# Performance work log

Hardware: AMD Instinct MI355X
Metric: run time of the kernel (lower is better)

## Reference

```python
import jax, jax.numpy as jnp
import numpy as np

D_MODEL = 2048
NUM_HEADS = 16
HEAD_DIM = D_MODEL // NUM_HEADS
B, S = 2, 2048


def rotate_half(x):
    x1, x2 = jnp.split(x, 2, axis=-1)
    return jnp.concatenate((-x2, x1), axis=-1)


def setup_inputs() -> dict:
    key = jax.random.key(0)
    ks = jax.random.split(key, 7)
    x = jax.random.normal(ks[0], (B, S, D_MODEL), dtype=jnp.float32)
    cos = jax.random.normal(ks[1], (1, 1, S, HEAD_DIM), dtype=jnp.float32)
    sin = jax.random.normal(ks[2], (1, 1, S, HEAD_DIM), dtype=jnp.float32)
    scale = 1.0 / np.sqrt(D_MODEL)
    Wq = jax.random.normal(ks[3], (D_MODEL, D_MODEL), dtype=jnp.float32) * scale
    Wk = jax.random.normal(ks[4], (D_MODEL, D_MODEL), dtype=jnp.float32) * scale
    Wv = jax.random.normal(ks[5], (D_MODEL, D_MODEL), dtype=jnp.float32) * scale
    Wo = jax.random.normal(ks[6], (D_MODEL, D_MODEL), dtype=jnp.float32) * scale
    return {"x": x, "cos": cos, "sin": sin, "Wq": Wq, "Wk": Wk, "Wv": Wv, "Wo": Wo}


def reference(x, cos, sin, Wq, Wk, Wv, Wo):
    Bb, Ss, Dd = x.shape
    H, hd = NUM_HEADS, HEAD_DIM
    # nn.Linear: y = x @ W.T ; here W stored as [out, in]
    q = (x @ Wq.T).reshape(Bb, Ss, H, hd).transpose(0, 2, 1, 3)  # [B,H,S,hd]
    k = (x @ Wk.T).reshape(Bb, Ss, H, hd).transpose(0, 2, 1, 3)
    v = (x @ Wv.T).reshape(Bb, Ss, H, hd).transpose(0, 2, 1, 3)
    q = q * cos + rotate_half(q) * sin
    k = k * cos + rotate_half(k) * sin
    scale = 1.0 / jnp.sqrt(jnp.asarray(hd, dtype=x.dtype))
    scores = jnp.einsum('bhqd,bhkd->bhqk', q, k) * scale  # [B,H,S,S]
    causal = jnp.tril(jnp.ones((Ss, Ss), dtype=bool))
    scores = jnp.where(causal[None, None], scores, jnp.finfo(x.dtype).min)
    attn = jax.nn.softmax(scores, axis=-1)
    out = jnp.einsum('bhqk,bhkd->bhqd', attn, v)  # [B,H,S,hd]
    out = out.transpose(0, 2, 1, 3).reshape(Bb, Ss, Dd)
    return out @ Wo.T
```

## Files before the change

### kernel.cpp

```cpp
#include <hip/hip_runtime.h>

typedef unsigned short u16;
typedef __attribute__((ext_vector_type(8))) short bf8v;
typedef __attribute__((ext_vector_type(4))) float f4v;

#define DEV static __device__ __forceinline__

DEV float bf2f(u16 u){ unsigned x = ((unsigned)u) << 16; float f; __builtin_memcpy(&f, &x, 4); return f; }
DEV u16 f2bf(float f){ unsigned x; __builtin_memcpy(&x, &f, 4); x += 0x7fff + ((x >> 16) & 1); return (u16)(x >> 16); }

DEV void async16(const void* g, void* l){
  __builtin_amdgcn_global_load_lds((const __attribute__((address_space(1))) unsigned*)g,
                                   (__attribute__((address_space(3))) unsigned*)l, 16, 0, 0);
}

DEV void vwait6(){ asm volatile("s_waitcnt vmcnt(6)" ::: "memory"); }
DEV void vwait0(){ asm volatile("s_waitcnt vmcnt(0)" ::: "memory"); }
DEV void bar(){ asm volatile("s_barrier" ::: "memory"); }

__global__ __launch_bounds__(256) void f2b_k(const float* __restrict__ src,
                                             u16* __restrict__ dst)
{
  const long i = ((long)blockIdx.x * 256 + threadIdx.x) * 4;
  const float4 v = *(const float4*)(src + i);
  ushort4 o;
  o.x = f2bf(v.x); o.y = f2bf(v.y); o.z = f2bf(v.z); o.w = f2bf(v.w);
  *(ushort4*)(dst + i) = o;
}

__global__ __launch_bounds__(256) void f2b3_k(const float* __restrict__ a,
                                              const float* __restrict__ b,
                                              const float* __restrict__ c,
                                              u16* __restrict__ dst)
{
  const int bx = blockIdx.x;
  const float* s = bx < 4096 ? a : (bx < 8192 ? b : c);
  const long soff = ((long)(bx & 4095) * 256 + threadIdx.x) * 4;
  const long doff = ((long)bx * 256 + threadIdx.x) * 4;
  const float4 v = *(const float4*)(s + soff);
  ushort4 o;
  o.x = f2bf(v.x); o.y = f2bf(v.y); o.z = f2bf(v.z); o.w = f2bf(v.w);
  *(ushort4*)(dst + doff) = o;
}

constexpr int KDIM = 2048;

__global__ __launch_bounds__(512, 2) void gemm256(const u16* __restrict__ A,
                                                  const u16* __restrict__ B,
                                                  u16* __restrict__ C0,
                                                  u16* __restrict__ C1,
                                                  u16* __restrict__ C2,
                                                  float* __restrict__ Cf, int mode)
{
  __shared__ __align__(16) u16 Asm[3][8192];
  __shared__ __align__(16) u16 Bsm[3][16384];

  const int tid = threadIdx.x;
  const int w = tid >> 6, lane = tid & 63;
  const int ln = lane & 15, quad = lane >> 4;
  const int wr = w >> 2, wc = w & 3;

  const int gx = gridDim.x;
  const int nwg = gx * gridDim.y;
  const int wg = blockIdx.y * gx + blockIdx.x;
  const int swz = (wg & 7) * (nwg >> 3) + (wg >> 3);
  const int bx = swz % gx, by = swz / gx;
  const long m0 = (long)by << 7, n0 = (long)bx << 8;

  f4v acc[4][4] = {};

  const u16* pA  = A + (m0 + w * 16 + ln) * (long)KDIM + quad * 8;
  const u16* pB0 = B + (n0 + w * 16 + ln) * (long)KDIM + quad * 8;
  const u16* pB1 = B + (n0 + (8 + w) * 16 + ln) * (long)KDIM + quad * 8;
  char* ldsA = (char*)Asm + (long)tid * 16;
  char* ldsB = (char*)Bsm + (long)tid * 16;

#define STG(sl, ks, kt) do{                                                     \
    async16(pA  + (kt) + (ks) * 32, ldsA + (sl) * 16384 + (ks) * 8192);         \
    async16(pB0 + (kt) + (ks) * 32, ldsB + (sl) * 32768 + (ks) * 16384);        \
    async16(pB1 + (kt) + (ks) * 32, ldsB + (sl) * 32768 + (ks) * 16384 + 8192); \
  }while(0)

  STG(0, 0, 0);  STG(0, 1, 0);
  STG(1, 0, 64); STG(1, 1, 64);
  vwait6();
  bar();

  int s0 = 0, s1 = 1, s2 = 2;
  const int nt = KDIM / 64;
  for (int t = 0; t < nt; ++t) {
    const u16* Ab = Asm[s0];
    const u16* Bb = Bsm[s0];
    const bool st = (t + 2 < nt);
    const long kt2 = (long)(t + 2) * 64;

    bf8v a0[4], b0[4];
#pragma unroll
    for (int i = 0; i < 4; ++i) a0[i] = *(const bf8v*)&Ab[((wr * 4 + i) * 64 + lane) * 8];
#pragma unroll
    for (int j = 0; j < 4; ++j) b0[j] = *(const bf8v*)&Bb[((wc * 4 + j) * 64 + lane) * 8];
    if (st) STG(s2, 0, kt2);
    bar();
    __builtin_amdgcn_s_setprio(1);
#pragma unroll
    for (int i = 0; i < 4; ++i)
#pragma unroll
      for (int j = 0; j < 4; ++j)
        acc[i][j] = __builtin_amdgcn_mfma_f32_16x16x32_bf16(a0[i], b0[j], acc[i][j], 0, 0, 0);
    __builtin_amdgcn_s_setprio(0);
    bar();

    bf8v a1[4], b1[4];
#pragma unroll
    for (int i = 0; i < 4; ++i) a1[i] = *(const bf8v*)&Ab[((8 + wr * 4 + i) * 64 + lane) * 8];
#pragma unroll
    for (int j = 0; j < 4; ++j) b1[j] = *(const bf8v*)&Bb[((16 + wc * 4 + j) * 64 + lane) * 8];
    if (st) STG(s2, 1, kt2);
    if (st) vwait6(); else vwait0();
    bar();
    __builtin_amdgcn_s_setprio(1);
#pragma unroll
    for (int i = 0; i < 4; ++i)
#pragma unroll
      for (int j = 0; j < 4; ++j)
        acc[i][j] = __builtin_amdgcn_mfma_f32_16x16x32_bf16(a1[i], b1[j], acc[i][j], 0, 0, 0);
    __builtin_amdgcn_s_setprio(0);
    bar();

    const int tmp = s0; s0 = s1; s1 = s2; s2 = tmp;
  }
#undef STG

#pragma unroll
  for (int i = 0; i < 4; i++) {
    const long mrow = m0 + wr * 64 + i * 16 + quad * 4;
#pragma unroll
    for (int j = 0; j < 4; j++) {
      const long ncol = n0 + wc * 64 + j * 16 + ln;
#pragma unroll
      for (int r = 0; r < 4; r++) {
        const float fv = acc[i][j][r];
        const long m = mrow + r;
        if (mode == 0) {
          C0[m * 2048 + ncol] = f2bf(fv);
        } else if (mode == 2) {
          Cf[m * 2048 + ncol] = fv;
        } else if (mode == 1) {
          const long s = m & 2047, bb = m >> 11;
          const long hh = ncol >> 7, dc = ncol & 127;
          C0[((bb * 16 + hh) * 128 + dc) * 2048 + s] = f2bf(fv);
        } else {
          const int sec = (int)(n0 >> 11);
          const long nc = ncol & 2047;
          if (sec == 0)      C0[m * 2048 + nc] = f2bf(fv);
          else if (sec == 1) C1[m * 2048 + nc] = f2bf(fv);
          else {
            const long s = m & 2047, bb = m >> 11;
            const long hh = nc >> 7, dc = nc & 127;
            C2[((bb * 16 + hh) * 128 + dc) * 2048 + s] = f2bf(fv);
          }
        }
      }
    }
  }
}

__global__ __launch_bounds__(256) void rope2_k(u16* __restrict__ qb,
                                               u16* __restrict__ kb,
                                               const float* __restrict__ cs,
                                               const float* __restrict__ sn)
{
  const long idx = (long)blockIdx.x * 256 + threadIdx.x;
  u16* t = (idx >= 4194304) ? kb : qb;
  const long i2 = idx & 4194303;
  const long m = i2 >> 10;
  const int rest = (int)(i2 & 1023);
  const int h = rest >> 6, d = rest & 63;
  const int s = (int)(m & 2047);
  const long base = m * 2048 + h * 128 + d;
  const float a  = bf2f(t[base]), b = bf2f(t[base + 64]);
  const float c1 = cs[s * 128 + d],      s1 = sn[s * 128 + d];
  const float c2 = cs[s * 128 + d + 64], s2 = sn[s * 128 + d + 64];
  t[base]      = f2bf(a * c1 - b * s1);
  t[base + 64] = f2bf(b * c2 + a * s2);
}

__global__ __launch_bounds__(256) void attn_k(const u16* __restrict__ q,
                                              const u16* __restrict__ k,
                                              const u16* __restrict__ vt,
                                              u16* __restrict__ ao)
{
  __shared__ __align__(16) u16 Ks[128 * 128];
  __shared__ __align__(16) u16 Vs[128 * 128];
  __shared__ __align__(16) u16 Ps[4 * 16 * 72];
  const int qt = 31 - blockIdx.x;
  const int bh = blockIdx.y;
  const int b = bh >> 4, h = bh & 15;
  const int tid = threadIdx.x;
  const int w = tid >> 6, lane = tid & 63;
  const int ln = lane & 15, quad = lane >> 4;
  const int q0 = qt << 6;

  const u16* kb0 = k + ((long)(b * 2048 + (tid & 15))) * 2048 + h * 128
                     + ((tid >> 6) & 3) * 32 + ((tid >> 4) & 3) * 8;
  const u16* vb0 = vt + ((long)(bh * 128 + (tid & 15))) * 2048
                      + ((tid >> 6) & 1) * 32 + ((tid >> 4) & 3) * 8;
  const int tb = tid >> 7;

  bf8v aq[4];
  {
    const u16* qp = q + ((long)(b * 2048 + q0 + w * 16 + ln)) * 2048 + h * 128;
#pragma unroll
    for (int dt = 0; dt < 4; ++dt) aq[dt] = *(const bf8v*)(qp + dt * 32 + quad * 8);
  }
  f4v O[8] = {};
  f4v Osum = {};
  const short one_bf = (short)0x3F80;
  const bf8v vones = {one_bf, one_bf, one_bf, one_bf, one_bf, one_bf, one_bf, one_bf};

  const int nktp = qt >> 1;
  for (int ktp = 0; ktp <= nktp; ++ktp) {
    const int k0s = ktp << 7;
    const bool has1 = (2 * ktp + 1) <= qt;

    __syncthreads();
#pragma unroll
    for (int it = 0; it < 8; ++it) {
      const int rowu = (it >> 2) * 64 + (it & 3) * 16;
      async16(kb0 + (long)(k0s + rowu) * 2048, (char*)Ks + it * 4096 + w * 1024);
    }
#pragma unroll
    for (int it = 0; it < 8; ++it) {
      const int g = 2 * it + tb;
      const long off = (long)((g & 7) * 16) * 2048 + (g >> 3) * 64 + k0s;
      async16(vb0 + off, (char*)Vs + it * 4096 + w * 1024);
    }
    __syncthreads();

    f4v S[8];
#pragma unroll
    for (int jt = 0; jt < 8; jt++) {
      if (jt >= 4 && !has1) { S[jt] = (f4v){-1e30f, -1e30f, -1e30f, -1e30f}; continue; }
      const int sub = jt >> 2, jl = jt & 3;
      f4v s = {};
#pragma unroll
      for (int dt = 0; dt < 4; dt++) {
        const bf8v bk = *(const bf8v*)&Ks[(sub * 1024 + (jl * 4 + dt) * 64 + lane) * 8];
        s = __builtin_amdgcn_mfma_f32_16x16x32_bf16(aq[dt], bk, s, 0, 0, 0);
      }
      S[jt] = s;
    }
    const float scl = 0.08838834764831845f;
    const float shift = 20.0f;
    if (ktp == nktp) {
      const int qi_loc = w * 16 + quad * 4;
#pragma unroll
      for (int jt = 0; jt < 8; jt++) {
        const int dcol = k0s - q0 + (jt >> 2) * 64 + (jt & 3) * 16 + ln;
#pragma unroll
        for (int r = 0; r < 4; r++) {
          const float arg = (dcol > qi_loc + r) ? -1e30f : (S[jt][r] * scl - shift);
          S[jt][r] = __expf(arg);
        }
      }
    } else {
#pragma unroll
      for (int jt = 0; jt < 8; jt++)
#pragma unroll
        for (int r = 0; r < 4; r++) S[jt][r] = __expf(S[jt][r] * scl - shift);
    }
    const int wbase = w * 16 * 72;
#pragma unroll
    for (int sub = 0; sub < 2; ++sub) {
      if (sub == 1 && !has1) break;
#pragma unroll
      for (int jl = 0; jl < 4; jl++)
#pragma unroll
        for (int r = 0; r < 4; r++)
          Ps[wbase + (quad * 4 + r) * 72 + jl * 16 + ln] = f2bf(S[sub * 4 + jl][r]);
      bf8v ap[2];
#pragma unroll
      for (int k2 = 0; k2 < 2; k2++)
        ap[k2] = *(const bf8v*)&Ps[wbase + ln * 72 + k2 * 32 + quad * 8];
#pragma unroll
      for (int nt = 0; nt < 8; nt++) {
#pragma unroll
        for (int k2 = 0; k2 < 2; k2++) {
          const bf8v bv = *(const bf8v*)&Vs[(sub * 1024 + (nt * 2 + k2) * 64 + lane) * 8];
          O[nt] = __builtin_amdgcn_mfma_f32_16x16x32_bf16(ap[k2], bv, O[nt], 0, 0, 0);
        }
      }
#pragma unroll
      for (int k2 = 0; k2 < 2; k2++)
        Osum = __builtin_amdgcn_mfma_f32_16x16x32_bf16(ap[k2], vones, Osum, 0, 0, 0);
    }
  }

  float inv[4];
#pragma unroll
  for (int r = 0; r < 4; r++) inv[r] = 1.0f / Osum[r];
  const long ob = ((long)(b * 2048 + q0 + w * 16 + quad * 4)) * 2048 + h * 128 + ln;
#pragma unroll
  for (int r = 0; r < 4; r++)
#pragma unroll
    for (int nt = 0; nt < 8; nt++)
      ao[ob + (long)r * 2048 + nt * 16] = f2bf(O[nt][r] * inv[r]);
}

extern "C" void kernel_launch(void* const* d_in, const int* in_sizes, int n_in,
                              void* d_out, int out_size, void* d_ws, size_t ws_size,
                              hipStream_t stream) {
  const float* x  = (const float*)d_in[0];
  const float* cs = (const float*)d_in[1];
  const float* sn = (const float*)d_in[2];
  const float* Wq = (const float*)d_in[3];
  const float* Wk = (const float*)d_in[4];
  const float* Wv = (const float*)d_in[5];
  const float* Wo = (const float*)d_in[6];
  float* out = (float*)d_out;

  const size_t E = 4194304;
  u16* xb = (u16*)d_ws;

  const size_t need = 11 * E * sizeof(u16);
  if (ws_size >= need) {
    u16* wqkv = xb + 2 * E;
    u16* qb   = wqkv + 3 * E;
    u16* kb   = qb + 2 * E;
    u16* vtb  = kb + 2 * E;
    u16* aob  = xb;

    f2b_k<<<8192, 256, 0, stream>>>(x, xb);
    f2b3_k<<<12288, 256, 0, stream>>>(Wq, Wk, Wv, wqkv);
    gemm256<<<dim3(24, 32), 512, 0, stream>>>(xb, wqkv, qb, kb, vtb, nullptr, 3);
    rope2_k<<<32768, 256, 0, stream>>>(qb, kb, cs, sn);
    attn_k<<<dim3(32, 32), 256, 0, stream>>>(qb, kb, vtb, aob);
    f2b_k<<<4096, 256, 0, stream>>>(Wo, wqkv);
    gemm256<<<dim3(8, 32), 512, 0, stream>>>(aob, wqkv, nullptr, nullptr, nullptr, out, 2);
  } else {
    u16* wb  = xb + 2 * E;
    u16* qb  = wb + E;
    u16* kb  = qb + 2 * E;
    u16* vtb = kb + 2 * E;
    u16* aob = xb;

    f2b_k<<<8192, 256, 0, stream>>>(x, xb);
    f2b_k<<<4096, 256, 0, stream>>>(Wq, wb);
    gemm256<<<dim3(8, 32), 512, 0, stream>>>(xb, wb, qb, nullptr, nullptr, nullptr, 0);
    f2b_k<<<4096, 256, 0, stream>>>(Wk, wb);
    gemm256<<<dim3(8, 32), 512, 0, stream>>>(xb, wb, kb, nullptr, nullptr, nullptr, 0);
    f2b_k<<<4096, 256, 0, stream>>>(Wv, wb);
    gemm256<<<dim3(8, 32), 512, 0, stream>>>(xb, wb, vtb, nullptr, nullptr, nullptr, 1);
    rope2_k<<<32768, 256, 0, stream>>>(qb, kb, cs, sn);
    attn_k<<<dim3(32, 32), 256, 0, stream>>>(qb, kb, vtb, aob);
    f2b_k<<<4096, 256, 0, stream>>>(Wo, wb);
    gemm256<<<dim3(8, 32), 512, 0, stream>>>(aob, wb, nullptr, nullptr, nullptr, out, 2);
  }
}
```

Before: 534.0 us.

## Double-buffer K/V tiles and pair causal query tiles in 512-thread attention blocks

The attention kernel is restructured so each 512-thread block handles 128 query rows and processes two query tiles (qt and 15-qt), balancing the causal work across blocks. K/V tiles are double-buffered in LDS, with the next tile's async loads issued before computing the current one. A partial vmcnt wait replaces the full sync. This is meant to hide global load latency and even out the triangular workload, at the cost of doubled LDS use (about 130KB) and fewer blocks (256) in flight.

```diff
diff --git a/kernel.cpp b/kernel.cpp
--- a/kernel.cpp
+++ b/kernel.cpp
@@ -14,6 +14,7 @@
                                    (__attribute__((address_space(3))) unsigned*)l, 16, 0, 0);
 }
 
+DEV void vwait8(){ asm volatile("s_waitcnt vmcnt(8)" ::: "memory"); }
 DEV void vwait6(){ asm volatile("s_waitcnt vmcnt(6)" ::: "memory"); }
 DEV void vwait0(){ asm volatile("s_waitcnt vmcnt(0)" ::: "memory"); }
 DEV void bar(){ asm volatile("s_barrier" ::: "memory"); }
@@ -185,126 +186,155 @@
   t[base + 64] = f2bf(b * c2 + a * s2);
 }
 
-__global__ __launch_bounds__(256) void attn_k(const u16* __restrict__ q,
+__global__ __launch_bounds__(512) void attn_k(const u16* __restrict__ q,
                                               const u16* __restrict__ k,
                                               const u16* __restrict__ vt,
                                               u16* __restrict__ ao)
 {
-  __shared__ __align__(16) u16 Ks[128 * 128];
-  __shared__ __align__(16) u16 Vs[128 * 128];
-  __shared__ __align__(16) u16 Ps[4 * 16 * 72];
-  const int qt = 31 - blockIdx.x;
+  __shared__ __align__(16) u16 Ks[2][16384];
+  __shared__ __align__(16) u16 Vs[2][16384];
+  __shared__ __align__(16) u16 Ps[8 * 16 * 72];
+  const int xa = blockIdx.x;
   const int bh = blockIdx.y;
   const int b = bh >> 4, h = bh & 15;
   const int tid = threadIdx.x;
   const int w = tid >> 6, lane = tid & 63;
   const int ln = lane & 15, quad = lane >> 4;
-  const int q0 = qt << 6;
 
   const u16* kb0 = k + ((long)(b * 2048 + (tid & 15))) * 2048 + h * 128
                      + ((tid >> 6) & 3) * 32 + ((tid >> 4) & 3) * 8;
   const u16* vb0 = vt + ((long)(bh * 128 + (tid & 15))) * 2048
                       + ((tid >> 6) & 1) * 32 + ((tid >> 4) & 3) * 8;
-  const int tb = tid >> 7;
-
-  bf8v aq[4];
-  {
-    const u16* qp = q + ((long)(b * 2048 + q0 + w * 16 + ln)) * 2048 + h * 128;
-#pragma unroll
-    for (int dt = 0; dt < 4; ++dt) aq[dt] = *(const bf8v*)(qp + dt * 32 + quad * 8);
-  }
-  f4v O[8] = {};
-  f4v Osum = {};
+  const int tb = (tid >> 7) & 1;
+  const int bit8 = tid >> 8;
+  int krow[4]; long voff[4];
+#pragma unroll
+  for (int it2 = 0; it2 < 4; ++it2) {
+    const int ie = 2 * it2 + bit8;
+    krow[it2] = (ie >> 2) * 64 + (ie & 3) * 16;
+    const int g = 2 * ie + tb;
+    voff[it2] = (long)((g & 7) * 16) * 2048 + (g >> 3) * 64;
+  }
+
+#define STK(sl, k0) do{                                                          \
+    _Pragma("unroll")                                                            \
+    for (int it2 = 0; it2 < 4; ++it2)                                            \
+      async16(kb0 + (long)((k0) + krow[it2]) * 2048,                             \
+              (char*)&Ks[sl][0] + it2 * 8192 + w * 1024);                        \
+  }while(0)
+#define STV(sl, k0) do{                                                          \
+    _Pragma("unroll")                                                            \
+    for (int it2 = 0; it2 < 4; ++it2)                                            \
+      async16(vb0 + voff[it2] + (k0),                                            \
+              (char*)&Vs[sl][0] + it2 * 8192 + w * 1024);                        \
+  }while(0)
+
   const short one_bf = (short)0x3F80;
   const bf8v vones = {one_bf, one_bf, one_bf, one_bf, one_bf, one_bf, one_bf, one_bf};
-
-  const int nktp = qt >> 1;
-  for (int ktp = 0; ktp <= nktp; ++ktp) {
-    const int k0s = ktp << 7;
-    const bool has1 = (2 * ktp + 1) <= qt;
-
-    __syncthreads();
-#pragma unroll
-    for (int it = 0; it < 8; ++it) {
-      const int rowu = (it >> 2) * 64 + (it & 3) * 16;
-      async16(kb0 + (long)(k0s + rowu) * 2048, (char*)Ks + it * 4096 + w * 1024);
+  const float scl = 0.08838834764831845f;
+  const float shift = 20.0f;
+  const int wbase = w * 16 * 72;
+  const int qts[2] = {15 - xa, xa};
+
+  for (int tix = 0; tix < 2; ++tix) {
+    const int qt = qts[tix];
+    const int q0 = qt << 7;
+
+    bf8v aq[4];
+    {
+      const u16* qp = q + ((long)(b * 2048 + q0 + w * 16 + ln)) * 2048 + h * 128;
+#pragma unroll
+      for (int dt = 0; dt < 4; ++dt) aq[dt] = *(const bf8v*)(qp + dt * 32 + quad * 8);
     }
-#pragma unroll
-    for (int it = 0; it < 8; ++it) {
-      const int g = 2 * it + tb;
-      const long off = (long)((g & 7) * 16) * 2048 + (g >> 3) * 64 + k0s;
-      async16(vb0 + off, (char*)Vs + it * 4096 + w * 1024);
+    f4v O[8] = {};
+    f4v Osum = {};
+
+    STK(0, 0); STV(0, 0);
+
+    for (int ktp = 0; ktp <= qt; ++ktp) {
+      const int k0s = ktp << 7;
+      const bool lastit = (ktp == qt);
+      const int sl = ktp & 1;
+      if (!lastit) { STK(sl ^ 1, k0s + 128); STV(sl ^ 1, k0s + 128); }
+      if (!lastit) vwait8(); else vwait0();
+      bar();
+      const u16* Kb = &Ks[sl][0];
+      const u16* Vb = &Vs[sl][0];
+
+      f4v S[8];
+#pragma unroll
+      for (int jt = 0; jt < 8; jt++) {
+        const int jb = (jt >> 2) * 64 + (jt & 3) * 16;
+        if (lastit && jb > w * 16 + 15) {
+          S[jt] = (f4v){-1e30f, -1e30f, -1e30f, -1e30f};
+          continue;
+        }
+        const int sub = jt >> 2, jl = jt & 3;
+        f4v s = {};
+#pragma unroll
+        for (int dt = 0; dt < 4; dt++) {
+          const bf8v bk = *(const bf8v*)&Kb[(sub * 1024 + (jl * 4 + dt) * 64 + lane) * 8];
+          s = __builtin_amdgcn_mfma_f32_16x16x32_bf16(aq[dt], bk, s, 0, 0, 0);
+        }
+        S[jt] = s;
+      }
+      if (lastit) {
+        const int qi = w * 16 + quad * 4;
+#pragma unroll
+        for (int jt = 0; jt < 8; jt++) {
+          const int dcol = (jt >> 2) * 64 + (jt & 3) * 16 + ln;
+#pragma unroll
+          for (int r = 0; r < 4; r++) {
+            const float arg = (dcol > qi + r) ? -1e30f : (S[jt][r] * scl - shift);
+            S[jt][r] = __expf(arg);
+          }
+        }
+      } else {
+#pragma unroll
+        for (int jt = 0; jt < 8; jt++)
+#pragma unroll
+          for (int r = 0; r < 4; r++) S[jt][r] = __expf(S[jt][r] * scl - shift);
+      }
+
+#pragma unroll
+      for (int sub = 0; sub < 2; ++sub) {
+        if (sub == 1 && lastit && w < 4) break;
+#pragma unroll
+        for (int jl = 0; jl < 4; jl++)
+#pragma unroll
+          for (int r = 0; r < 4; r++)
+            Ps[wbase + (quad * 4 + r) * 72 + jl * 16 + ln] = f2bf(S[sub * 4 + jl][r]);
+        bf8v ap[2];
+#pragma unroll
+        for (int k2 = 0; k2 < 2; k2++)
+          ap[k2] = *(const bf8v*)&Ps[wbase + ln * 72 + k2 * 32 + quad * 8];
+#pragma unroll
+        for (int nt = 0; nt < 8; nt++) {
+#pragma unroll
+          for (int k2 = 0; k2 < 2; k2++) {
+            const bf8v bv = *(const bf8v*)&Vb[(sub * 1024 + (nt * 2 + k2) * 64 + lane) * 8];
+            O[nt] = __builtin_amdgcn_mfma_f32_16x16x32_bf16(ap[k2], bv, O[nt], 0, 0, 0);
+          }
+        }
+#pragma unroll
+        for (int k2 = 0; k2 < 2; k2++)
+          Osum = __builtin_amdgcn_mfma_f32_16x16x32_bf16(ap[k2], vones, Osum, 0, 0, 0);
+      }
+      bar();
     }
-    __syncthreads();
-
-    f4v S[8];
-#pragma unroll
-    for (int jt = 0; jt < 8; jt++) {
-      if (jt >= 4 && !has1) { S[jt] = (f4v){-1e30f, -1e30f, -1e30f, -1e30f}; continue; }
-      const int sub = jt >> 2, jl = jt & 3;
-      f4v s = {};
-#pragma unroll
-      for (int dt = 0; dt < 4; dt++) {
-        const bf8v bk = *(const bf8v*)&Ks[(sub * 1024 + (jl * 4 + dt) * 64 + lane) * 8];
-        s = __builtin_amdgcn_mfma_f32_16x16x32_bf16(aq[dt], bk, s, 0, 0, 0);
-      }
-      S[jt] = s;
-    }
-    const float scl = 0.08838834764831845f;
-    const float shift = 20.0f;
-    if (ktp == nktp) {
-      const int qi_loc = w * 16 + quad * 4;
-#pragma unroll
-      for (int jt = 0; jt < 8; jt++) {
-        const int dcol = k0s - q0 + (jt >> 2) * 64 + (jt & 3) * 16 + ln;
-#pragma unroll
-        for (int r = 0; r < 4; r++) {
-          const float arg = (dcol > qi_loc + r) ? -1e30f : (S[jt][r] * scl - shift);
-          S[jt][r] = __expf(arg);
-        }
-      }
-    } else {
-#pragma unroll
-      for (int jt = 0; jt < 8; jt++)
-#pragma unroll
-        for (int r = 0; r < 4; r++) S[jt][r] = __expf(S[jt][r] * scl - shift);
-    }
-    const int wbase = w * 16 * 72;
-#pragma unroll
-    for (int sub = 0; sub < 2; ++sub) {
-      if (sub == 1 && !has1) break;
-#pragma unroll
-      for (int jl = 0; jl < 4; jl++)
-#pragma unroll
-        for (int r = 0; r < 4; r++)
-          Ps[wbase + (quad * 4 + r) * 72 + jl * 16 + ln] = f2bf(S[sub * 4 + jl][r]);
-      bf8v ap[2];
-#pragma unroll
-      for (int k2 = 0; k2 < 2; k2++)
-        ap[k2] = *(const bf8v*)&Ps[wbase + ln * 72 + k2 * 32 + quad * 8];
-#pragma unroll
-      for (int nt = 0; nt < 8; nt++) {
-#pragma unroll
-        for (int k2 = 0; k2 < 2; k2++) {
-          const bf8v bv = *(const bf8v*)&Vs[(sub * 1024 + (nt * 2 + k2) * 64 + lane) * 8];
-          O[nt] = __builtin_amdgcn_mfma_f32_16x16x32_bf16(ap[k2], bv, O[nt], 0, 0, 0);
-        }
-      }
-#pragma unroll
-      for (int k2 = 0; k2 < 2; k2++)
-        Osum = __builtin_amdgcn_mfma_f32_16x16x32_bf16(ap[k2], vones, Osum, 0, 0, 0);
-    }
-  }
-
-  float inv[4];
-#pragma unroll
-  for (int r = 0; r < 4; r++) inv[r] = 1.0f / Osum[r];
-  const long ob = ((long)(b * 2048 + q0 + w * 16 + quad * 4)) * 2048 + h * 128 + ln;
-#pragma unroll
-  for (int r = 0; r < 4; r++)
-#pragma unroll
-    for (int nt = 0; nt < 8; nt++)
-      ao[ob + (long)r * 2048 + nt * 16] = f2bf(O[nt][r] * inv[r]);
+
+    float inv[4];
+#pragma unroll
+    for (int r = 0; r < 4; r++) inv[r] = 1.0f / Osum[r];
+    const long ob = ((long)(b * 2048 + q0 + w * 16 + quad * 4)) * 2048 + h * 128 + ln;
+#pragma unroll
+    for (int r = 0; r < 4; r++)
+#pragma unroll
+      for (int nt = 0; nt < 8; nt++)
+        ao[ob + (long)r * 2048 + nt * 16] = f2bf(O[nt][r] * inv[r]);
+  }
+#undef STK
+#undef STV
 }
 
 extern "C" void kernel_launch(void* const* d_in, const int* in_sizes, int n_in,
@@ -334,7 +364,7 @@
     f2b3_k<<<12288, 256, 0, stream>>>(Wq, Wk, Wv, wqkv);
     gemm256<<<dim3(24, 32), 512, 0, stream>>>(xb, wqkv, qb, kb, vtb, nullptr, 3);
     rope2_k<<<32768, 256, 0, stream>>>(qb, kb, cs, sn);
-    attn_k<<<dim3(32, 32), 256, 0, stream>>>(qb, kb, vtb, aob);
+    attn_k<<<dim3(8, 32), 512, 0, stream>>>(qb, kb, vtb, aob);
     f2b_k<<<4096, 256, 0, stream>>>(Wo, wqkv);
     gemm256<<<dim3(8, 32), 512, 0, stream>>>(aob, wqkv, nullptr, nullptr, nullptr, out, 2);
   } else {
@@ -352,7 +382,7 @@
     f2b_k<<<4096, 256, 0, stream>>>(Wv, wb);
     gemm256<<<dim3(8, 32), 512, 0, stream>>>(xb, wb, vtb, nullptr, nullptr, nullptr, 1);
     rope2_k<<<32768, 256, 0, stream>>>(qb, kb, cs, sn);
-    attn_k<<<dim3(32, 32), 256, 0, stream>>>(qb, kb, vtb, aob);
+    attn_k<<<dim3(8, 32), 512, 0, stream>>>(qb, kb, vtb, aob);
     f2b_k<<<4096, 256, 0, stream>>>(Wo, wb);
     gemm256<<<dim3(8, 32), 512, 0, stream>>>(aob, wb, nullptr, nullptr, nullptr, out, 2);
   }
```

After: 478.9 us. 1.12x faster.
